# Kernel optimization log

Hardware: AMD Instinct MI355X
Metric: run time of the kernel (lower is better)

The kernel has to match this reference:

```python
import jax, jax.numpy as jnp
import numpy as np

B, L_Q, S_KV, H, E = 4, 1024, 1024, 8, 64
IN_CH = OUT_CH = 512
MODES = 64
INDEX_Q = np.arange(MODES)   # 'lowest' mode selection -> range(0, modes)
INDEX_KV = np.arange(MODES)
SCALE = 1.0 / np.sqrt(OUT_CH)
FACTOR = 5


def setup_inputs() -> dict:
    key = jax.random.key(0)
    ks = jax.random.split(key, 7)
    tf_queries = jax.random.normal(ks[0], (B, L_Q, H, E), jnp.float32)
    queries = jax.random.normal(ks[1], (B, L_Q, H, E), jnp.float32)
    keys = jax.random.normal(ks[2], (B, S_KV, H, E), jnp.float32)
    values = jax.random.normal(ks[3], (B, S_KV, H, E), jnp.float32)
    mask = jnp.ones((1,), jnp.int32)  # unused by the module
    weights_fuse = jax.random.uniform(ks[4], (H, L_Q, 2), jnp.float32)
    # torch.rand with cfloat dtype samples re/im independently from U[0,1)
    w1_re = SCALE * jax.random.uniform(ks[5], (H, IN_CH // 8, OUT_CH // 8, MODES), jnp.float32)
    w1_im = SCALE * jax.random.uniform(ks[6], (H, IN_CH // 8, OUT_CH // 8, MODES), jnp.float32)
    return dict(tf_queries=tf_queries, queries=queries, keys=keys, values=values,
                mask=mask, weights_fuse=weights_fuse, w1_re=w1_re, w1_im=w1_im)


def get_sig_scores(n, queries, keys, scale, corr):
    # queries/keys: [B, L, H, E] (keys already aligned to L_Q)
    B_, Lq, H_, E_ = queries.shape
    Lk = keys.shape[1]
    q = jnp.transpose(queries, (0, 2, 1, 3))  # [B,H,L,E]
    k = jnp.transpose(keys, (0, 2, 1, 3))
    if corr:
        qf = jnp.fft.rfft(jnp.transpose(queries, (0, 2, 3, 1)), axis=-1)
        kf = jnp.fft.rfft(jnp.transpose(keys, (0, 2, 3, 1)), axis=-1)
        autocorr = jnp.transpose(jnp.fft.irfft(qf * jnp.conj(kf), axis=-1), (0, 1, 3, 2))  # [B,H,L,E]
    else:
        autocorr = q
    amp = jnp.linalg.norm(autocorr, axis=-1)           # [B,H,L]
    _, top_idx = jax.lax.top_k(amp, n)                 # [B,H,n]
    q_sel = jnp.take_along_axis(q, top_idx[..., None], axis=2)  # [B,H,n,E]
    scores = jnp.einsum('bhnd,bhmd->bhnm', q_sel, k) * scale    # [B,H,n,Lk]
    full = jnp.full((B_, H_, Lq, Lk), -jnp.inf, scores.dtype)
    bi = jnp.arange(B_)[:, None, None]
    hi = jnp.arange(H_)[None, :, None]
    full = full.at[bi, hi, top_idx].set(scores)        # scatter selected query rows
    # softmax over the query axis for every key position (transpose(2,3))
    return jax.nn.softmax(jnp.swapaxes(full, 2, 3), axis=-1)  # [B,H,Lk,Lq]


def reference(tf_queries, queries, keys, values, mask, weights_fuse, w1_re, w1_im):
    B_, Lq, H_, E_ = queries.shape
    S_ = keys.shape[1]
    xq = jnp.transpose(queries, (0, 2, 3, 1))  # [B,H,E,L_Q]
    xk = jnp.transpose(keys, (0, 2, 3, 1))     # [B,H,E,S]
    if Lq > S_:
        pad = jnp.zeros((B_, Lq - S_, H_, E_), keys.dtype)
        keys2 = jnp.concatenate([keys, pad], axis=1)
        values2 = jnp.concatenate([values, pad], axis=1)
    else:
        keys2 = keys[:, :Lq]
        values2 = values[:, :Lq]
    n_top = min(int(FACTOR * np.ceil(np.log(Lq))), Lq)

    attn_t = get_sig_scores(n_top, queries, keys2, SCALE, corr=True)
    attn_tf = get_sig_scores(n_top, tf_queries, keys2, SCALE, corr=False)

    nw = jax.nn.softmax(weights_fuse, axis=-1)  # [H,L_Q,2]
    fused = nw[None, :, :, 0, None] * attn_t + nw[None, :, :, 1, None] * attn_tf
    # dropout(p=0.1) in eval mode -> identity

    xq_ft = jnp.fft.rfft(xq, axis=-1)[:, :, :, INDEX_Q]   # [B,H,E,M]
    xk_ft = jnp.fft.rfft(xk, axis=-1)[:, :, :, INDEX_KV]  # [B,H,E,M]
    xqk = jnp.tanh(jnp.einsum('bhex,bhey->bhxy', xq_ft, xk_ft))  # complex tanh
    xqkv = jnp.einsum('bhxy,bhey->bhex', xqk, xk_ft)
    w1 = w1_re + 1j * w1_im
    xqkvw = jnp.einsum('bhex,heox->bhox', xqkv, w1)        # [B,H,O,M]
    out_ft = jnp.zeros((B_, H_, E_, Lq // 2 + 1), xqkvw.dtype)
    out_ft = out_ft.at[:, :, :, INDEX_Q].set(xqkvw)
    out = jnp.fft.irfft(out_ft / IN_CH / OUT_CH, n=Lq, axis=-1)  # [B,H,E,L_Q]

    output = jnp.einsum('bhlm,bhmd->bhld', fused, jnp.transpose(values2, (0, 2, 1, 3)))
    output = jnp.transpose(output, (0, 1, 3, 2))  # [B,H,D,L_Q]
    return (output + out) * 0.5
```

## Files before the change

### kernel.cpp

```cpp
#include <hip/hip_runtime.h>
#include <math.h>

#define B_ 4
#define H_ 8
#define L_ 1024
#define E_ 64
#define NTOP 35
#define SCALE_ 0.04419417382415922f


__device__ __forceinline__ void dev_stage(char* smem, int vbid,
                                          const float* __restrict__ q_g,
                                          const float* __restrict__ k_g,
                                          float* __restrict__ xtq,
                                          float* __restrict__ xtk) {
  float* tile = reinterpret_cast<float*>(smem);
  const int tc = vbid & 15;
  const int src = (vbid >> 4) & 1;
  const int bh = vbid >> 5;
  const int b = bh >> 3, h = bh & 7;
  const int t0 = tc * 64;
  const int tid = threadIdx.x;
  const float* in = src ? k_g : q_g;
  float* out = src ? xtk : xtq;

  for (int idx = tid; idx < 1024; idx += 256) {
    int t = idx >> 4, e4 = idx & 15;
    float4 v = reinterpret_cast<const float4*>(
        in + ((size_t)(b * L_ + t0 + t) * H_ + h) * E_)[e4];
    tile[t * 65 + e4 * 4 + 0] = v.x; tile[t * 65 + e4 * 4 + 1] = v.y;
    tile[t * 65 + e4 * 4 + 2] = v.z; tile[t * 65 + e4 * 4 + 3] = v.w;
  }
  __syncthreads();
  for (int idx = tid; idx < 1024; idx += 256) {
    int e = idx >> 4, t4 = idx & 15;
    float4 v = make_float4(tile[(t4 * 4 + 0) * 65 + e], tile[(t4 * 4 + 1) * 65 + e],
                           tile[(t4 * 4 + 2) * 65 + e], tile[(t4 * 4 + 3) * 65 + e]);
    reinterpret_cast<float4*>(out + ((size_t)(bh * 64 + e)) * 1024 + t0)[t4] = v;
  }
}

__device__ __forceinline__ void dev_tfqnorm(int vbid,
                                            const float* __restrict__ tfq,
                                            float* __restrict__ ampsum) {
  const int bh = vbid >> 2, qt = vbid & 3;
  const int b = bh >> 3, h = bh & 7;
  const int l = qt * 256 + threadIdx.x;
  const float4* p4 = reinterpret_cast<const float4*>(
      &tfq[((size_t)(b * L_ + l) * H_ + h) * E_]);
  float s = 0.f;
#pragma unroll
  for (int e4 = 0; e4 < 16; ++e4) {
    float4 v = p4[e4];
    s += v.x * v.x + v.y * v.y + v.z * v.z + v.w * v.w;
  }
  ampsum[(size_t)(bh * 2 + 1) * 1024 + l] = s;
}

__device__ __forceinline__ void dev_fft(char* smem, int vbid,
                                        const float* __restrict__ xtq,
                                        const float* __restrict__ xtk,
                                        float* __restrict__ amp2_part,
                                        float* __restrict__ qft,
                                        float* __restrict__ kft) {
  float* zre = reinterpret_cast<float*>(smem);
  float* zim = zre + 4096;
  float* ctab = zim + 4096;
  float* stab = ctab + 512;
  const int eg = vbid & 15;
  const int bh = vbid >> 4;
  const int tid = threadIdx.x;
  const float TWO_PI_N = 6.283185307179586f / 1024.0f;

  if (tid < 512) {
    float s, c;
    sincosf(TWO_PI_N * (float)tid, &s, &c);
    ctab[tid] = c; stab[tid] = s;
  }
  for (int idx = tid; idx < 1024; idx += 512) {
    int ee = idx >> 8, t4 = idx & 255;
    size_t ro = ((size_t)(bh * 64 + eg * 4 + ee)) * 1024;
    float4 qv = reinterpret_cast<const float4*>(xtq + ro)[t4];
    float4 kv = reinterpret_cast<const float4*>(xtk + ro)[t4];
    *reinterpret_cast<float4*>(&zre[ee * 1024 + t4 * 4]) = qv;
    *reinterpret_cast<float4*>(&zim[ee * 1024 + t4 * 4]) = kv;
  }
  __syncthreads();

  for (int s = 0; s < 10; ++s) {
    const int half = 512 >> s;
#pragma unroll
    for (int it = 0; it < 4; ++it) {
      int idx = tid + it * 512;
      int ee = idx >> 9;
      int bf = idx & 511;
      int j = bf & (half - 1);
      int p0 = ((bf >> (9 - s)) << (10 - s)) + j;
      int p1 = p0 + half;
      float ur = zre[ee * 1024 + p0], ui = zim[ee * 1024 + p0];
      float vr = zre[ee * 1024 + p1], vi = zim[ee * 1024 + p1];
      float dr = ur - vr, di = ui - vi;
      zre[ee * 1024 + p0] = ur + vr; zim[ee * 1024 + p0] = ui + vi;
      int twi = j << s;
      float c = ctab[twi], sn = stab[twi];
      zre[ee * 1024 + p1] = fmaf(dr, c, di * sn);
      zim[ee * 1024 + p1] = fmaf(di, c, -dr * sn);
    }
    __syncthreads();
  }

  float pr[8], pi_[8];
#pragma unroll
  for (int it = 0; it < 8; ++it) {
    int idx = tid + it * 512;
    int ee = idx >> 10;
    int p = idx & 1023;
    int m = __brev((unsigned)p) >> 22;
    int mp = (1024 - m) & 1023;
    int pp = __brev((unsigned)mp) >> 22;
    float ar = zre[ee * 1024 + p], ai = zim[ee * 1024 + p];
    float br = zre[ee * 1024 + pp], bi = zim[ee * 1024 + pp];
    float qr = 0.5f * (ar + br), qi = 0.5f * (ai - bi);
    float kr = 0.5f * (ai + bi), ki = -0.5f * (ar - br);
    pr[it]  = fmaf(qr, kr, qi * ki);
    pi_[it] = fmaf(qi, kr, -qr * ki);
    if (m < 64) {
      size_t o = ((size_t)(bh * 64 + eg * 4 + ee) * 64 + m) * 2;
      qft[o] = qr; qft[o + 1] = qi;
      kft[o] = kr; kft[o + 1] = ki;
    }
  }
  __syncthreads();
#pragma unroll
  for (int it = 0; it < 8; ++it) {
    int idx = tid + it * 512;
    int ee = idx >> 10;
    int p = idx & 1023;
    zre[ee * 1024 + p] = pr[it]; zim[ee * 1024 + p] = pi_[it];
  }
  __syncthreads();

  for (int idx = tid; idx < 2048; idx += 512) {
    int u = idx >> 10;
    int p = idx & 1023;
    int e0 = 2 * u, e1 = 2 * u + 1;
    float s_r = zre[e0 * 1024 + p] - zim[e1 * 1024 + p];
    float s_i = zim[e0 * 1024 + p] + zre[e1 * 1024 + p];
    zre[e0 * 1024 + p] = s_r; zim[e0 * 1024 + p] = s_i;
  }
  __syncthreads();

  for (int s = 9; s >= 0; --s) {
    const int half = 512 >> s;
#pragma unroll
    for (int it = 0; it < 2; ++it) {
      int idx = tid + it * 512;
      int ee = (idx >> 9) * 2;
      int bf = idx & 511;
      int j = bf & (half - 1);
      int p0 = ((bf >> (9 - s)) << (10 - s)) + j;
      int p1 = p0 + half;
      int twi = j << s;
      float c = ctab[twi], sn = stab[twi];
      float ur = zre[ee * 1024 + p0], ui = zim[ee * 1024 + p0];
      float wr = zre[ee * 1024 + p1], wi = zim[ee * 1024 + p1];
      float vr = fmaf(wr, c, -wi * sn);
      float vi = fmaf(wi, c, wr * sn);
      zre[ee * 1024 + p0] = ur + vr; zim[ee * 1024 + p0] = ui + vi;
      zre[ee * 1024 + p1] = ur - vr; zim[ee * 1024 + p1] = ui - vi;
    }
    __syncthreads();
  }

  for (int t = tid; t < 1024; t += 512) {
    float r0 = zre[t], i0 = zim[t];
    float r2 = zre[2 * 1024 + t], i2 = zim[2 * 1024 + t];
    amp2_part[(size_t)(bh * 16 + eg) * 1024 + t] =
        fmaf(r0, r0, fmaf(i0, i0, fmaf(r2, r2, i2 * i2)));
  }
}

__device__ __forceinline__ void dev_sel(char* smem, int vbid,
                                        const float* __restrict__ amp2_part,
                                        const float* __restrict__ ampsum,
                                        int* __restrict__ sel_ws) {
  float* amp = reinterpret_cast<float*>(smem);
  const int p = vbid;
  const int tid = threadIdx.x;

  if ((p & 1) == 0) {
    const int bh = p >> 1;
    for (int t = tid; t < 1024; t += 256) {
      float s = 0.f;
#pragma unroll
      for (int c = 0; c < 16; ++c)
        s += amp2_part[(size_t)(bh * 16 + c) * 1024 + t];
      amp[t] = s;
    }
  } else {
    for (int t = tid; t < 1024; t += 256)
      amp[t] = ampsum[(size_t)p * 1024 + t];
  }
  __syncthreads();

  if (tid < 64) {
    const int lane = tid;
    float val[16];
#pragma unroll
    for (int j = 0; j < 16; ++j) val[j] = amp[j * 64 + lane];

    float bv = -1.f; int bi = lane;
#pragma unroll
    for (int j = 0; j < 16; ++j) {
      if (val[j] > bv) { bv = val[j]; bi = j * 64 + lane; }
    }
    for (int it = 0; it < NTOP; ++it) {
      float v = bv; int i = bi;
#pragma unroll
      for (int d = 1; d < 64; d <<= 1) {
        float ov = __shfl_xor(v, d);
        int oi = __shfl_xor(i, d);
        if (ov > v || (ov == v && oi < i)) { v = ov; i = oi; }
      }
      if (lane == 0) sel_ws[p * 64 + it] = i;
      if ((i & 63) == lane) {
        int jr = i >> 6;
#pragma unroll
        for (int j = 0; j < 16; ++j) if (j == jr) val[j] = -1.f;
        bv = -1.f; bi = lane;
#pragma unroll
        for (int j = 0; j < 16; ++j) {
          if (val[j] > bv) { bv = val[j]; bi = j * 64 + lane; }
        }
      }
    }
  }
}

__device__ __forceinline__ void dev_attn(char* smem, int vbid,
                                         const float* __restrict__ q_g,
                                         const float* __restrict__ tfq,
                                         const float* __restrict__ k_g,
                                         const float* __restrict__ v_g,
                                         const float* __restrict__ wfuse,
                                         const int* __restrict__ sel_ws,
                                         float* __restrict__ out) {
  float4* qs4 = reinterpret_cast<float4*>(smem);
  float4* vs4 = qs4 + 2 * NTOP * 16;
  const int ac = vbid & 15;
  const int bh = vbid >> 4;
  const int b = bh >> 3, h = bh & 7;
  const int a0 = ac * 64;
  const int tid = threadIdx.x;

  for (int idx = tid; idx < 2 * NTOP * 16; idx += 256) {
    int src = idx / (NTOP * 16);
    int rem = idx - src * (NTOP * 16);
    int i = rem >> 4, e4 = rem & 15;
    int row = sel_ws[(bh * 2 + src) * 64 + i];
    size_t rb = ((size_t)(b * L_ + row) * H_ + h) * E_;
    const float* qbase = src ? tfq : q_g;
    qs4[(src * NTOP + i) * 16 + e4] = reinterpret_cast<const float4*>(qbase + rb)[e4];
    vs4[(src * NTOP + i) * 16 + e4] = reinterpret_cast<const float4*>(v_g + rb)[e4];
  }
  __syncthreads();

  const int qd = tid & 3, r = tid >> 2;
  const int a = a0 + r;
  const int eb = qd * 16;

  size_t krb = ((size_t)(b * L_ + a) * H_ + h) * E_;
  const float4* k4p = reinterpret_cast<const float4*>(k_g + krb);
  float4 kq[4];
#pragma unroll
  for (int j4 = 0; j4 < 4; ++j4) kq[j4] = k4p[qd * 4 + j4];

  float ct[NTOP], ctf[NTOP];
#pragma unroll
  for (int i = 0; i < NTOP; ++i) { ct[i] = 0.f; ctf[i] = 0.f; }

#pragma unroll
  for (int j4 = 0; j4 < 4; ++j4) {
    float4 kv = kq[j4];
#pragma unroll
    for (int i = 0; i < NTOP; ++i) {
      float4 q4 = qs4[(0 * NTOP + i) * 16 + qd * 4 + j4];
      ct[i] = fmaf(q4.x, kv.x, ct[i]); ct[i] = fmaf(q4.y, kv.y, ct[i]);
      ct[i] = fmaf(q4.z, kv.z, ct[i]); ct[i] = fmaf(q4.w, kv.w, ct[i]);
      float4 p4 = qs4[(1 * NTOP + i) * 16 + qd * 4 + j4];
      ctf[i] = fmaf(p4.x, kv.x, ctf[i]); ctf[i] = fmaf(p4.y, kv.y, ctf[i]);
      ctf[i] = fmaf(p4.z, kv.z, ctf[i]); ctf[i] = fmaf(p4.w, kv.w, ctf[i]);
    }
  }
#pragma unroll
  for (int i = 0; i < NTOP; ++i) {
    ct[i] += __shfl_xor(ct[i], 1);  ct[i] += __shfl_xor(ct[i], 2);
    ctf[i] += __shfl_xor(ctf[i], 1); ctf[i] += __shfl_xor(ctf[i], 2);
  }

  float wf0 = wfuse[(h * L_ + a) * 2 + 0];
  float wf1 = wfuse[(h * L_ + a) * 2 + 1];
  float wm = fmaxf(wf0, wf1);
  float ew0 = expf(wf0 - wm), ew1 = expf(wf1 - wm);
  float nw0 = ew0 / (ew0 + ew1), nw1 = ew1 / (ew0 + ew1);

  {
    float m = -1e30f;
#pragma unroll
    for (int i = 0; i < NTOP; ++i) { ct[i] *= SCALE_; m = fmaxf(m, ct[i]); }
    float sum = 0.f;
#pragma unroll
    for (int i = 0; i < NTOP; ++i) { ct[i] = expf(ct[i] - m); sum += ct[i]; }
    float c = 0.5f * nw0 / sum;
#pragma unroll
    for (int i = 0; i < NTOP; ++i) ct[i] *= c;
  }
  {
    float m = -1e30f;
#pragma unroll
    for (int i = 0; i < NTOP; ++i) { ctf[i] *= SCALE_; m = fmaxf(m, ctf[i]); }
    float sum = 0.f;
#pragma unroll
    for (int i = 0; i < NTOP; ++i) { ctf[i] = expf(ctf[i] - m); sum += ctf[i]; }
    float c = 0.5f * nw1 / sum;
#pragma unroll
    for (int i = 0; i < NTOP; ++i) ctf[i] *= c;
  }
#pragma unroll
  for (int j4 = 0; j4 < 4; ++j4) {
    float ax = 0.f, ay = 0.f, az = 0.f, aw = 0.f;
#pragma unroll
    for (int i = 0; i < NTOP; ++i) {
      float4 v4 = vs4[(0 * NTOP + i) * 16 + qd * 4 + j4];
      ax = fmaf(ct[i], v4.x, ax); ay = fmaf(ct[i], v4.y, ay);
      az = fmaf(ct[i], v4.z, az); aw = fmaf(ct[i], v4.w, aw);
    }
#pragma unroll
    for (int i = 0; i < NTOP; ++i) {
      float4 v4 = vs4[(1 * NTOP + i) * 16 + qd * 4 + j4];
      ax = fmaf(ctf[i], v4.x, ax); ay = fmaf(ctf[i], v4.y, ay);
      az = fmaf(ctf[i], v4.z, az); aw = fmaf(ctf[i], v4.w, aw);
    }
    int d = eb + j4 * 4;
    out[((size_t)(bh * 64 + d + 0)) * 1024 + a] = ax;
    out[((size_t)(bh * 64 + d + 1)) * 1024 + a] = ay;
    out[((size_t)(bh * 64 + d + 2)) * 1024 + a] = az;
    out[((size_t)(bh * 64 + d + 3)) * 1024 + a] = aw;
  }
}

__device__ __forceinline__ void dev_spec12(char* smem, int vbid,
                                           const float* __restrict__ qft,
                                           const float* __restrict__ kft,
                                           float* __restrict__ xre_g,
                                           float* __restrict__ xim_g) {
  float* kre = reinterpret_cast<float*>(smem);
  float* kim = kre + 4160;
  float* qre = kim + 4160;
  float* qim = qre + 512;
  float* tre = qim + 512;
  float* tim = tre + 512;
  const int xc = vbid & 7;
  const int bh = vbid >> 3;
  const int tid = threadIdx.x;

  for (int idx = tid; idx < 4096; idx += 256) {
    int e = idx >> 6, y = idx & 63;
    size_t o = ((size_t)(bh * 64 + e) * 64 + y) * 2;
    kre[e * 65 + y] = kft[o]; kim[e * 65 + y] = kft[o + 1];
  }
  for (int idx = tid; idx < 512; idx += 256) {
    int e = idx >> 3, xl = idx & 7;
    size_t o = ((size_t)(bh * 64 + e) * 64 + xc * 8 + xl) * 2;
    qre[e * 8 + xl] = qft[o]; qim[e * 8 + xl] = qft[o + 1];
  }
  __syncthreads();

  const int y = tid & 63, xg = tid >> 6;
#pragma unroll
  for (int xi = 0; xi < 2; ++xi) {
    int xl = xg + xi * 4;
    float ar = 0.f, ai = 0.f;
    for (int e = 0; e < 64; ++e) {
      float a = qre[e * 8 + xl], b = qim[e * 8 + xl];
      float c = kre[e * 65 + y], d = kim[e * 65 + y];
      ar = fmaf(a, c, fmaf(-b, d, ar));
      ai = fmaf(a, d, fmaf(b, c, ai));
    }
    float trv, tiv;
    float x2 = 2.f * ar, y2 = 2.f * ai;
    if (fabsf(x2) > 30.f) {
      trv = copysignf(1.f, ar); tiv = 0.f;
    } else {
      float sh = sinhf(x2), ch = coshf(x2);
      float sn = sinf(y2), cs = cosf(y2);
      float dd = ch + cs;
      trv = sh / dd; tiv = sn / dd;
    }
    tre[xl * 64 + y] = trv; tim[xl * 64 + y] = tiv;
  }
  __syncthreads();

  const int e2 = tid & 63, xg2 = tid >> 6;
#pragma unroll
  for (int xi = 0; xi < 2; ++xi) {
    int xl = xg2 + xi * 4;
    float ar = 0.f, ai = 0.f;
    for (int yy = 0; yy < 64; ++yy) {
      float a = tre[xl * 64 + yy], b = tim[xl * 64 + yy];
      float c = kre[e2 * 65 + yy], d = kim[e2 * 65 + yy];
      ar = fmaf(a, c, fmaf(-b, d, ar));
      ai = fmaf(a, d, fmaf(b, c, ai));
    }
    xre_g[(size_t)bh * 4096 + (xc * 8 + xl) * 64 + e2] = ar;
    xim_g[(size_t)bh * 4096 + (xc * 8 + xl) * 64 + e2] = ai;
  }
}

__device__ __forceinline__ void dev_w1(char* smem, int vbid,
                                       const float* __restrict__ xre_g,
                                       const float* __restrict__ xim_g,
                                       const float* __restrict__ w1re,
                                       const float* __restrict__ w1im,
                                       float* __restrict__ xw) {
  float* xre = reinterpret_cast<float*>(smem);
  float* xim = xre + 4160;
  const int oc = vbid & 7;
  const int bh = vbid >> 3;
  const int h = bh & 7;
  const int tid = threadIdx.x;

  for (int idx = tid; idx < 4096; idx += 256) {
    int x = idx >> 6, e = idx & 63;
    xre[e * 65 + x] = xre_g[(size_t)bh * 4096 + idx];
    xim[e * 65 + x] = xim_g[(size_t)bh * 4096 + idx];
  }
  __syncthreads();

  const int x = tid & 63, g = tid >> 6;
  const int o0 = oc * 8 + g * 2;
  float ar0 = 0.f, ai0 = 0.f, ar1 = 0.f, ai1 = 0.f;
  for (int e = 0; e < 64; ++e) {
    float a = xre[e * 65 + x], b = xim[e * 65 + x];
    size_t wb = (((size_t)h * 64 + e) * 64 + o0) * 64 + x;
    float c0 = w1re[wb], d0 = w1im[wb];
    float c1 = w1re[wb + 64], d1 = w1im[wb + 64];
    ar0 = fmaf(a, c0, fmaf(-b, d0, ar0));
    ai0 = fmaf(a, d0, fmaf(b, c0, ai0));
    ar1 = fmaf(a, c1, fmaf(-b, d1, ar1));
    ai1 = fmaf(a, d1, fmaf(b, c1, ai1));
  }
  const float INV = 1.0f / (512.0f * 512.0f);
  size_t oidx0 = ((size_t)(bh * 64 + o0) * 64 + x) * 2;
  xw[oidx0] = ar0 * INV; xw[oidx0 + 1] = ai0 * INV;
  size_t oidx1 = ((size_t)(bh * 64 + o0 + 1) * 64 + x) * 2;
  xw[oidx1] = ar1 * INV; xw[oidx1 + 1] = ai1 * INV;
}

__device__ __forceinline__ void dev_final(char* smem, int vbid,
                                          const float* __restrict__ xw,
                                          float* __restrict__ out) {
  float* Xre = reinterpret_cast<float*>(smem);
  float* Xim = Xre + 512;
  const int tc = vbid & 3;
  const int oc = (vbid >> 2) & 7;
  const int bh = vbid >> 5;
  const int o0 = oc * 8;
  const int tid = threadIdx.x;

  for (int idx = tid; idx < 512; idx += 256) {
    int o = idx >> 6, m = idx & 63;
    size_t s = ((size_t)(bh * 64 + o0 + o) * 64 + m) * 2;
    Xre[o * 64 + m] = 2.f * xw[s]; Xim[o * 64 + m] = 2.f * xw[s + 1];
  }
  __syncthreads();

  const int t = tc * 256 + tid;
  const float HALF_INVN = 0.5f / 1024.0f;
  const float TWO_PI = 6.283185307179586f;
  float th = TWO_PI * (float)t * (1.0f / 1024.0f);
  float s1, c1;
  __sincosf(th, &s1, &c1);
  float cm = c1, sm = s1;

  float acc[8];
#pragma unroll
  for (int o = 0; o < 8; ++o) acc[o] = 0.5f * Xre[o * 64];

  for (int m = 1; m < 64; ++m) {
#pragma unroll
    for (int o = 0; o < 8; ++o) {
      acc[o] = fmaf(Xre[o * 64 + m], cm, acc[o]);
      acc[o] = fmaf(-Xim[o * 64 + m], sm, acc[o]);
    }
    float cn = fmaf(cm, c1, -sm * s1);
    float sn = fmaf(sm, c1, cm * s1);
    cm = cn; sm = sn;
  }
#pragma unroll
  for (int o = 0; o < 8; ++o) {
    size_t oi = ((size_t)(bh * 64 + o0 + o)) * 1024 + t;
    out[oi] = fmaf(acc[o], HALF_INVN, out[oi]);
  }
}


__global__ __launch_bounds__(256) void k_L1(const float* __restrict__ q,
                                            const float* __restrict__ k,
                                            const float* __restrict__ tfq,
                                            float* __restrict__ xtq,
                                            float* __restrict__ xtk,
                                            float* __restrict__ ampsum) {
  __shared__ __align__(16) char smem[16640];
  if (blockIdx.x < 1024) dev_stage(smem, blockIdx.x, q, k, xtq, xtk);
  else dev_tfqnorm(blockIdx.x - 1024, tfq, ampsum);
}

__global__ __launch_bounds__(512) void k_L2(const float* __restrict__ xtq,
                                            const float* __restrict__ xtk,
                                            float* __restrict__ amp2,
                                            float* __restrict__ qft,
                                            float* __restrict__ kft) {
  __shared__ __align__(16) char smem[36864];
  dev_fft(smem, blockIdx.x, xtq, xtk, amp2, qft, kft);
}

__global__ __launch_bounds__(256) void k_L3(const float* __restrict__ amp2,
                                            const float* __restrict__ ampsum,
                                            int* __restrict__ sel,
                                            const float* __restrict__ qft,
                                            const float* __restrict__ kft,
                                            float* __restrict__ xre_g,
                                            float* __restrict__ xim_g) {
  __shared__ __align__(16) char smem[41472];
  if (blockIdx.x < 64) dev_sel(smem, blockIdx.x, amp2, ampsum, sel);
  else dev_spec12(smem, blockIdx.x - 64, qft, kft, xre_g, xim_g);
}

__global__ __launch_bounds__(256) void k_L4(const float* __restrict__ q,
                                            const float* __restrict__ tfq,
                                            const float* __restrict__ k,
                                            const float* __restrict__ v,
                                            const float* __restrict__ wfuse,
                                            const int* __restrict__ sel,
                                            float* __restrict__ out,
                                            const float* __restrict__ xre_g,
                                            const float* __restrict__ xim_g,
                                            const float* __restrict__ w1re,
                                            const float* __restrict__ w1im,
                                            float* __restrict__ xw) {
  __shared__ __align__(16) char smem[35840];
  if (blockIdx.x < 512) dev_attn(smem, blockIdx.x, q, tfq, k, v, wfuse, sel, out);
  else dev_w1(smem, blockIdx.x - 512, xre_g, xim_g, w1re, w1im, xw);
}

__global__ __launch_bounds__(256) void k_L5(const float* __restrict__ xw,
                                            float* __restrict__ out) {
  __shared__ __align__(16) char smem[4096];
  dev_final(smem, blockIdx.x, xw, out);
}


__global__ __launch_bounds__(256) void k_fft_s(const float* __restrict__ q_g,
                                               const float* __restrict__ k_g,
                                               float* __restrict__ amp2_part,
                                               float* __restrict__ qft,
                                               float* __restrict__ kft) {
  __shared__ float zre[4][1024], zim[4][1024];
  __shared__ float ctab[512], stab[512];
  const int eg = blockIdx.x & 15;
  const int bh = blockIdx.x >> 4;
  const int b = bh >> 3, h = bh & 7;
  const int tid = threadIdx.x;
  const float TWO_PI_N = 6.283185307179586f / 1024.0f;

  for (int j = tid; j < 512; j += 256) {
    float s, c;
    sincosf(TWO_PI_N * (float)j, &s, &c);
    ctab[j] = c; stab[j] = s;
  }
  for (int t = tid; t < 1024; t += 256) {
    size_t g4 = ((size_t)(b * L_ + t) * H_ + h) * 16 + eg;
    float4 qv = reinterpret_cast<const float4*>(q_g)[g4];
    float4 kv = reinterpret_cast<const float4*>(k_g)[g4];
    zre[0][t] = qv.x; zre[1][t] = qv.y; zre[2][t] = qv.z; zre[3][t] = qv.w;
    zim[0][t] = kv.x; zim[1][t] = kv.y; zim[2][t] = kv.z; zim[3][t] = kv.w;
  }
  __syncthreads();

  for (int s = 0; s < 10; ++s) {
    const int half = 512 >> s;
#pragma unroll
    for (int it = 0; it < 8; ++it) {
      int idx = tid + it * 256;
      int ee = idx >> 9;
      int bf = idx & 511;
      int j = bf & (half - 1);
      int p0 = ((bf >> (9 - s)) << (10 - s)) + j;
      int p1 = p0 + half;
      float ur = zre[ee][p0], ui = zim[ee][p0];
      float vr = zre[ee][p1], vi = zim[ee][p1];
      float dr = ur - vr, di = ui - vi;
      zre[ee][p0] = ur + vr; zim[ee][p0] = ui + vi;
      int twi = j << s;
      float c = ctab[twi], sn = stab[twi];
      zre[ee][p1] = fmaf(dr, c, di * sn);
      zim[ee][p1] = fmaf(di, c, -dr * sn);
    }
    __syncthreads();
  }

  float pr[16], pi_[16];
#pragma unroll
  for (int it = 0; it < 16; ++it) {
    int idx = tid + it * 256;
    int ee = idx >> 10;
    int p = idx & 1023;
    int m = __brev((unsigned)p) >> 22;
    int mp = (1024 - m) & 1023;
    int pp = __brev((unsigned)mp) >> 22;
    float ar = zre[ee][p], ai = zim[ee][p];
    float br = zre[ee][pp], bi = zim[ee][pp];
    float qr = 0.5f * (ar + br), qi = 0.5f * (ai - bi);
    float kr = 0.5f * (ai + bi), ki = -0.5f * (ar - br);
    pr[it]  = fmaf(qr, kr, qi * ki);
    pi_[it] = fmaf(qi, kr, -qr * ki);
    if (m < 64) {
      size_t o = ((size_t)(bh * 64 + eg * 4 + ee) * 64 + m) * 2;
      qft[o] = qr; qft[o + 1] = qi;
      kft[o] = kr; kft[o + 1] = ki;
    }
  }
  __syncthreads();
#pragma unroll
  for (int it = 0; it < 16; ++it) {
    int idx = tid + it * 256;
    int ee = idx >> 10;
    int p = idx & 1023;
    zre[ee][p] = pr[it]; zim[ee][p] = pi_[it];
  }
  __syncthreads();

  for (int idx = tid; idx < 2048; idx += 256) {
    int u = idx >> 10;
    int p = idx & 1023;
    int e0 = 2 * u, e1 = 2 * u + 1;
    float s_r = zre[e0][p] - zim[e1][p];
    float s_i = zim[e0][p] + zre[e1][p];
    zre[e0][p] = s_r; zim[e0][p] = s_i;
  }
  __syncthreads();

  for (int s = 9; s >= 0; --s) {
    const int half = 512 >> s;
#pragma unroll
    for (int it = 0; it < 4; ++it) {
      int idx = tid + it * 256;
      int ee = (idx >> 9) * 2;
      int bf = idx & 511;
      int j = bf & (half - 1);
      int p0 = ((bf >> (9 - s)) << (10 - s)) + j;
      int p1 = p0 + half;
      int twi = j << s;
      float c = ctab[twi], sn = stab[twi];
      float ur = zre[ee][p0], ui = zim[ee][p0];
      float wr = zre[ee][p1], wi = zim[ee][p1];
      float vr = fmaf(wr, c, -wi * sn);
      float vi = fmaf(wi, c, wr * sn);
      zre[ee][p0] = ur + vr; zim[ee][p0] = ui + vi;
      zre[ee][p1] = ur - vr; zim[ee][p1] = ui - vi;
    }
    __syncthreads();
  }

  for (int t = tid; t < 1024; t += 256) {
    float r0 = zre[0][t], i0 = zim[0][t];
    float r2 = zre[2][t], i2 = zim[2][t];
    amp2_part[(size_t)(bh * 16 + eg) * 1024 + t] =
        fmaf(r0, r0, fmaf(i0, i0, fmaf(r2, r2, i2 * i2)));
  }
}

__global__ __launch_bounds__(256) void k_topk(const float* __restrict__ amp2_part,
                                              const float* __restrict__ tfq,
                                              int* __restrict__ sel_ws) {
  __shared__ float amp[1024];
  __shared__ float wv_s[4];
  __shared__ int wi_s[4];
  __shared__ int winner_s;
  const int src = blockIdx.x & 1;
  const int bh = blockIdx.x >> 1;
  const int b = bh >> 3, h = bh & 7;
  const int tid = threadIdx.x;

  if (src == 0) {
    for (int t = tid; t < 1024; t += 256) {
      float s = 0.f;
#pragma unroll
      for (int c = 0; c < 16; ++c) s += amp2_part[(size_t)(bh * 16 + c) * 1024 + t];
      amp[t] = s;
    }
  } else {
    for (int l = tid; l < 1024; l += 256) {
      const float4* p4 = reinterpret_cast<const float4*>(
          &tfq[((size_t)(b * L_ + l) * H_ + h) * E_]);
      float s = 0.f;
#pragma unroll
      for (int e4 = 0; e4 < 16; ++e4) {
        float4 v = p4[e4];
        s += v.x * v.x + v.y * v.y + v.z * v.z + v.w * v.w;
      }
      amp[l] = s;
    }
  }
  __syncthreads();

  float bv = -1.f; int bi = tid;
#pragma unroll
  for (int kk = 0; kk < 4; ++kk) {
    int t = tid + kk * 256;
    float v = amp[t];
    if (v > bv) { bv = v; bi = t; }
  }
  const int lane = tid & 63, w = tid >> 6;

  for (int it = 0; it < NTOP; ++it) {
    float v = bv; int i = bi;
#pragma unroll
    for (int d = 1; d < 64; d <<= 1) {
      float ov = __shfl_xor(v, d);
      int oi = __shfl_xor(i, d);
      if (ov > v || (ov == v && oi < i)) { v = ov; i = oi; }
    }
    if (lane == 0) { wv_s[w] = v; wi_s[w] = i; }
    __syncthreads();
    if (tid == 0) {
      float fv = wv_s[0]; int fi = wi_s[0];
#pragma unroll
      for (int j = 1; j < 4; ++j) {
        if (wv_s[j] > fv || (wv_s[j] == fv && wi_s[j] < fi)) { fv = wv_s[j]; fi = wi_s[j]; }
      }
      winner_s = fi;
      sel_ws[(bh * 2 + src) * 64 + it] = fi;
    }
    __syncthreads();
    int fi = winner_s;
    if ((fi & 255) == tid) {
      amp[fi] = -1.f;
      bv = -1.f; bi = tid;
#pragma unroll
      for (int kk = 0; kk < 4; ++kk) {
        int t = tid + kk * 256;
        float vv = amp[t];
        if (vv > bv) { bv = vv; bi = t; }
      }
    }
  }
}

__global__ __launch_bounds__(256) void k_attn_w(const float* __restrict__ q,
                                                const float* __restrict__ tfq,
                                                const float* __restrict__ k,
                                                const float* __restrict__ v,
                                                const float* __restrict__ wfuse,
                                                const int* __restrict__ sel,
                                                float* __restrict__ out) {
  __shared__ __align__(16) char smem[35840];
  dev_attn(smem, blockIdx.x, q, tfq, k, v, wfuse, sel, out);
}

__global__ __launch_bounds__(256) void k_spec12_w(const float* __restrict__ qft,
                                                  const float* __restrict__ kft,
                                                  float* __restrict__ xre_g,
                                                  float* __restrict__ xim_g) {
  __shared__ __align__(16) char smem[41472];
  dev_spec12(smem, blockIdx.x, qft, kft, xre_g, xim_g);
}

__global__ __launch_bounds__(256) void k_w1_w(const float* __restrict__ xre_g,
                                              const float* __restrict__ xim_g,
                                              const float* __restrict__ w1re,
                                              const float* __restrict__ w1im,
                                              float* __restrict__ xw) {
  __shared__ __align__(16) char smem[33280];
  dev_w1(smem, blockIdx.x, xre_g, xim_g, w1re, w1im, xw);
}

extern "C" void kernel_launch(void* const* d_in, const int* in_sizes, int n_in,
                              void* d_out, int out_size, void* d_ws, size_t ws_size,
                              hipStream_t stream) {
  const float* tfq   = (const float*)d_in[0];
  const float* q     = (const float*)d_in[1];
  const float* k     = (const float*)d_in[2];
  const float* v     = (const float*)d_in[3];
  const float* wfuse = (const float*)d_in[5];
  const float* w1re  = (const float*)d_in[6];
  const float* w1im  = (const float*)d_in[7];
  float* out = (float*)d_out;
  float* ws  = (float*)d_ws;

  const size_t STAGED_FLOATS = 5312512;
  if (ws_size >= STAGED_FLOATS * sizeof(float)) {
    float* xtq    = ws;
    float* xtk    = ws + 2097152;
    float* amp2   = ws + 4194304;
    float* qft    = ws + 4718592;
    float* kft    = ws + 4980736;
    int*   sel    = (int*)(ws + 5242880);
    float* ampsum = ws + 5246976;
    float* xre_g  = ws;
    float* xim_g  = ws + 131072;
    float* xw     = ws + 262144;

    k_L1<<<1152, 256, 0, stream>>>(q, k, tfq, xtq, xtk, ampsum);
    k_L2<<<512, 512, 0, stream>>>(xtq, xtk, amp2, qft, kft);
    k_L3<<<320, 256, 0, stream>>>(amp2, ampsum, sel, qft, kft, xre_g, xim_g);
    k_L4<<<768, 256, 0, stream>>>(q, tfq, k, v, wfuse, sel, out,
                                  xre_g, xim_g, w1re, w1im, xw);
    k_L5<<<1024, 256, 0, stream>>>(xw, out);
  } else {
    float* amp2  = ws;
    float* xre_g = ws;
    float* xim_g = ws + 131072;
    float* xw    = ws + 262144;
    float* qft   = ws + 524288;
    float* kft   = ws + 786432;
    int*   sel   = (int*)(ws + 1048576);

    k_fft_s<<<512, 256, 0, stream>>>(q, k, amp2, qft, kft);
    k_topk<<<64, 256, 0, stream>>>(amp2, tfq, sel);
    k_attn_w<<<512, 256, 0, stream>>>(q, tfq, k, v, wfuse, sel, out);
    k_spec12_w<<<256, 256, 0, stream>>>(qft, kft, xre_g, xim_g);
    k_w1_w<<<256, 256, 0, stream>>>(xre_g, xim_g, w1re, w1im, xw);
    k_L5<<<1024, 256, 0, stream>>>(xw, out);
  }
}
```

Baseline: 114.0 us.

## Fuse five-stage pipeline into one persistent cooperative kernel with grid syncs

```diff
diff --git a/kernel.cpp b/kernel.cpp
--- a/kernel.cpp
+++ b/kernel.cpp
@@ -1,5 +1,8 @@
 #include <hip/hip_runtime.h>
+#include <hip/hip_cooperative_groups.h>
 #include <math.h>
+
+namespace cg = cooperative_groups;
 
 #define B_ 4
 #define H_ 8
@@ -57,12 +60,12 @@
   ampsum[(size_t)(bh * 2 + 1) * 1024 + l] = s;
 }
 
-__device__ __forceinline__ void dev_fft(char* smem, int vbid,
-                                        const float* __restrict__ xtq,
-                                        const float* __restrict__ xtk,
-                                        float* __restrict__ amp2_part,
-                                        float* __restrict__ qft,
-                                        float* __restrict__ kft) {
+__device__ __forceinline__ void dev_fft256(char* smem, int vbid,
+                                           const float* __restrict__ xtq,
+                                           const float* __restrict__ xtk,
+                                           float* __restrict__ amp2_part,
+                                           float* __restrict__ qft,
+                                           float* __restrict__ kft) {
   float* zre = reinterpret_cast<float*>(smem);
   float* zim = zre + 4096;
   float* ctab = zim + 4096;
@@ -72,12 +75,12 @@
   const int tid = threadIdx.x;
   const float TWO_PI_N = 6.283185307179586f / 1024.0f;
 
-  if (tid < 512) {
+  for (int j = tid; j < 512; j += 256) {
     float s, c;
-    sincosf(TWO_PI_N * (float)tid, &s, &c);
-    ctab[tid] = c; stab[tid] = s;
-  }
-  for (int idx = tid; idx < 1024; idx += 512) {
+    sincosf(TWO_PI_N * (float)j, &s, &c);
+    ctab[j] = c; stab[j] = s;
+  }
+  for (int idx = tid; idx < 1024; idx += 256) {
     int ee = idx >> 8, t4 = idx & 255;
     size_t ro = ((size_t)(bh * 64 + eg * 4 + ee)) * 1024;
     float4 qv = reinterpret_cast<const float4*>(xtq + ro)[t4];
@@ -90,8 +93,8 @@
   for (int s = 0; s < 10; ++s) {
     const int half = 512 >> s;
 #pragma unroll
-    for (int it = 0; it < 4; ++it) {
-      int idx = tid + it * 512;
+    for (int it = 0; it < 8; ++it) {
+      int idx = tid + it * 256;
       int ee = idx >> 9;
       int bf = idx & 511;
       int j = bf & (half - 1);
@@ -109,10 +112,10 @@
     __syncthreads();
   }
 
-  float pr[8], pi_[8];
-#pragma unroll
-  for (int it = 0; it < 8; ++it) {
-    int idx = tid + it * 512;
+  float pr[16], pi_[16];
+#pragma unroll
+  for (int it = 0; it < 16; ++it) {
+    int idx = tid + it * 256;
     int ee = idx >> 10;
     int p = idx & 1023;
     int m = __brev((unsigned)p) >> 22;
@@ -132,15 +135,15 @@
   }
   __syncthreads();
 #pragma unroll
-  for (int it = 0; it < 8; ++it) {
-    int idx = tid + it * 512;
+  for (int it = 0; it < 16; ++it) {
+    int idx = tid + it * 256;
     int ee = idx >> 10;
     int p = idx & 1023;
     zre[ee * 1024 + p] = pr[it]; zim[ee * 1024 + p] = pi_[it];
   }
   __syncthreads();
 
-  for (int idx = tid; idx < 2048; idx += 512) {
+  for (int idx = tid; idx < 2048; idx += 256) {
     int u = idx >> 10;
     int p = idx & 1023;
     int e0 = 2 * u, e1 = 2 * u + 1;
@@ -153,8 +156,8 @@
   for (int s = 9; s >= 0; --s) {
     const int half = 512 >> s;
 #pragma unroll
-    for (int it = 0; it < 2; ++it) {
-      int idx = tid + it * 512;
+    for (int it = 0; it < 4; ++it) {
+      int idx = tid + it * 256;
       int ee = (idx >> 9) * 2;
       int bf = idx & 511;
       int j = bf & (half - 1);
@@ -172,7 +175,7 @@
     __syncthreads();
   }
 
-  for (int t = tid; t < 1024; t += 512) {
+  for (int t = tid; t < 1024; t += 256) {
     float r0 = zre[t], i0 = zim[t];
     float r2 = zre[2 * 1024 + t], i2 = zim[2 * 1024 + t];
     amp2_part[(size_t)(bh * 16 + eg) * 1024 + t] =
@@ -505,6 +508,49 @@
 }
 
 
+__global__ __launch_bounds__(256) void k_mega(
+    const float* __restrict__ q, const float* __restrict__ k,
+    const float* __restrict__ tfq, const float* __restrict__ v,
+    const float* __restrict__ wfuse, const float* __restrict__ w1re,
+    const float* __restrict__ w1im, float* __restrict__ out,
+    float* __restrict__ xtq, float* __restrict__ xtk,
+    float* __restrict__ amp2, float* __restrict__ qft,
+    float* __restrict__ kft, int* __restrict__ sel,
+    float* __restrict__ ampsum, float* __restrict__ xw,
+    float* __restrict__ xre_g, float* __restrict__ xim_g) {
+  __shared__ __align__(16) char smem[41472];
+  cg::grid_group grid = cg::this_grid();
+
+  for (int vb = blockIdx.x; vb < 1152; vb += gridDim.x) {
+    if (vb < 1024) dev_stage(smem, vb, q, k, xtq, xtk);
+    else dev_tfqnorm(vb - 1024, tfq, ampsum);
+    __syncthreads();
+  }
+  grid.sync();
+  for (int vb = blockIdx.x; vb < 512; vb += gridDim.x) {
+    dev_fft256(smem, vb, xtq, xtk, amp2, qft, kft);
+    __syncthreads();
+  }
+  grid.sync();
+  for (int vb = blockIdx.x; vb < 320; vb += gridDim.x) {
+    if (vb < 64) dev_sel(smem, vb, amp2, ampsum, sel);
+    else dev_spec12(smem, vb - 64, qft, kft, xre_g, xim_g);
+    __syncthreads();
+  }
+  grid.sync();
+  for (int vb = blockIdx.x; vb < 768; vb += gridDim.x) {
+    if (vb < 512) dev_attn(smem, vb, q, tfq, k, v, wfuse, sel, out);
+    else dev_w1(smem, vb - 512, xre_g, xim_g, w1re, w1im, xw);
+    __syncthreads();
+  }
+  grid.sync();
+  for (int vb = blockIdx.x; vb < 1024; vb += gridDim.x) {
+    dev_final(smem, vb, xw, out);
+    __syncthreads();
+  }
+}
+
+
 __global__ __launch_bounds__(256) void k_L1(const float* __restrict__ q,
                                             const float* __restrict__ k,
                                             const float* __restrict__ tfq,
@@ -516,13 +562,13 @@
   else dev_tfqnorm(blockIdx.x - 1024, tfq, ampsum);
 }
 
-__global__ __launch_bounds__(512) void k_L2(const float* __restrict__ xtq,
+__global__ __launch_bounds__(256) void k_L2(const float* __restrict__ xtq,
                                             const float* __restrict__ xtk,
                                             float* __restrict__ amp2,
                                             float* __restrict__ qft,
                                             float* __restrict__ kft) {
   __shared__ __align__(16) char smem[36864];
-  dev_fft(smem, blockIdx.x, xtq, xtk, amp2, qft, kft);
+  dev_fft256(smem, blockIdx.x, xtq, xtk, amp2, qft, kft);
 }
 
 __global__ __launch_bounds__(256) void k_L3(const float* __restrict__ amp2,
@@ -559,7 +605,6 @@
   __shared__ __align__(16) char smem[4096];
   dev_final(smem, blockIdx.x, xw, out);
 }
-
 
 __global__ __launch_bounds__(256) void k_fft_s(const float* __restrict__ q_g,
                                                const float* __restrict__ k_g,
@@ -812,12 +857,36 @@
     float* xim_g  = ws + 131072;
     float* xw     = ws + 262144;
 
-    k_L1<<<1152, 256, 0, stream>>>(q, k, tfq, xtq, xtk, ampsum);
-    k_L2<<<512, 512, 0, stream>>>(xtq, xtk, amp2, qft, kft);
-    k_L3<<<320, 256, 0, stream>>>(amp2, ampsum, sel, qft, kft, xre_g, xim_g);
-    k_L4<<<768, 256, 0, stream>>>(q, tfq, k, v, wfuse, sel, out,
-                                  xre_g, xim_g, w1re, w1im, xw);
-    k_L5<<<1024, 256, 0, stream>>>(xw, out);
+    int dev = 0;
+    hipGetDevice(&dev);
+    int coop = 0;
+    hipDeviceGetAttribute(&coop, hipDeviceAttributeCooperativeLaunch, dev);
+    int ncu = 0;
+    hipDeviceGetAttribute(&ncu, hipDeviceAttributeMultiprocessorCount, dev);
+    int maxb = 0;
+    hipError_t oe = hipOccupancyMaxActiveBlocksPerMultiprocessor(
+        &maxb, (const void*)k_mega, 256, 0);
+
+    if (coop != 0 && oe == hipSuccess && maxb >= 1 && ncu >= 1) {
+      int grid = maxb * ncu;
+      if (grid > 1152) grid = 1152;
+      void* kp[18];
+      kp[0] = (void*)&q;      kp[1] = (void*)&k;      kp[2] = (void*)&tfq;
+      kp[3] = (void*)&v;      kp[4] = (void*)&wfuse;  kp[5] = (void*)&w1re;
+      kp[6] = (void*)&w1im;   kp[7] = (void*)&out;    kp[8] = (void*)&xtq;
+      kp[9] = (void*)&xtk;    kp[10] = (void*)&amp2;  kp[11] = (void*)&qft;
+      kp[12] = (void*)&kft;   kp[13] = (void*)&sel;   kp[14] = (void*)&ampsum;
+      kp[15] = (void*)&xw;    kp[16] = (void*)&xre_g; kp[17] = (void*)&xim_g;
+      hipLaunchCooperativeKernel((const void*)k_mega, dim3(grid), dim3(256),
+                                 kp, 0, stream);
+    } else {
+      k_L1<<<1152, 256, 0, stream>>>(q, k, tfq, xtq, xtk, ampsum);
+      k_L2<<<512, 256, 0, stream>>>(xtq, xtk, amp2, qft, kft);
+      k_L3<<<320, 256, 0, stream>>>(amp2, ampsum, sel, qft, kft, xre_g, xim_g);
+      k_L4<<<768, 256, 0, stream>>>(q, tfq, k, v, wfuse, sel, out,
+                                    xre_g, xim_g, w1re, w1im, xw);
+      k_L5<<<1024, 256, 0, stream>>>(xw, out);
+    }
   } else {
     float* amp2  = ws;
     float* xre_g = ws;
```

Result: slower. 120.9 us (+6.0%).
